# Performance work log

Hardware: AMD Instinct MI355X
Metric: run time of the kernel (lower is better)

## Reference

```python
import jax, jax.numpy as jnp
import numpy as np

B, S, D, H = 2, 2048, 1024, 16
DK = D // H

def setup_inputs() -> dict:
    key = jax.random.key(0)
    ks = jax.random.split(key, 12)
    def lin(k):
        kw, kb = jax.random.split(k)
        bound = 1.0 / np.sqrt(D)
        W = jax.random.uniform(kw, (D, D), jnp.float32, -bound, bound)
        b = jax.random.uniform(kb, (D,), jnp.float32, -bound, bound)
        return W, b
    Wq, bq = lin(ks[0]); Wk, bk = lin(ks[1]); Wv, bv = lin(ks[2]); Wo, bo = lin(ks[3])
    q = jax.random.normal(ks[4], (B, S, D), jnp.float32)
    k = jax.random.normal(ks[5], (B, S, D), jnp.float32)
    v = jax.random.normal(ks[6], (B, S, D), jnp.float32)
    mask = jnp.ones((1, 1, S, S), jnp.int32)
    return {"q": q, "k": k, "v": v, "mask": mask,
            "Wq": Wq, "bq": bq, "Wk": Wk, "bk": bk,
            "Wv": Wv, "bv": bv, "Wo": Wo, "bo": bo}

def reference(q, k, v, mask, Wq, bq, Wk, bk, Wv, bv, Wo, bo):
    # torch Linear: y = x @ W.T + b
    Q = (q @ Wq.T + bq).reshape(B, S, H, DK).transpose(0, 2, 1, 3)  # [B,H,S,DK]
    K = (k @ Wk.T + bk).reshape(B, S, H, DK).transpose(0, 2, 1, 3)
    V = (v @ Wv.T + bv).reshape(B, S, H, DK).transpose(0, 2, 1, 3)
    scores = jnp.einsum('bhqd,bhkd->bhqk', Q, K) / jnp.sqrt(jnp.float32(DK))
    scores = jnp.where(mask == 0, jnp.float32(-1e9), scores)
    attn = jax.nn.softmax(scores, axis=-1)
    context = jnp.einsum('bhqk,bhkd->bhqd', attn, V)  # [B,H,S,DK]
    concat = context.transpose(0, 2, 1, 3).reshape(B, S, D)
    return concat @ Wo.T + bo
```

## Files before the change

### kernel.cpp

```cpp
#include <hip/hip_runtime.h>
#include <hip/hip_bf16.h>

#define BB 2
#define SS 2048
#define DD 1024
#define HH 16
#define DKK 64

typedef __hip_bfloat16 bf16;
typedef unsigned short u16;
using frag_ab = __attribute__((ext_vector_type(8))) short;
using frag_cd = __attribute__((ext_vector_type(4))) float;

__device__ inline u16 f2bf(float f) {
    bf16 h = __float2bfloat16(f);
    return *reinterpret_cast<u16*>(&h);
}

__device__ inline void gld16(const void* g, void* l) {
    __builtin_amdgcn_global_load_lds((const __attribute__((address_space(1))) void*)g,
                                     (__attribute__((address_space(3))) void*)l,
                                     16, 0, 0);
}

__device__ inline int swz16(int idx) {
    return idx ^ (((idx >> 6) & 7) << 3);
}

__global__ __launch_bounds__(256) void prep(
    const float* __restrict__ q, const float* __restrict__ k, const float* __restrict__ v,
    const float* __restrict__ Wq, const float* __restrict__ Wk,
    const float* __restrict__ Wv, const float* __restrict__ Wo,
    u16* __restrict__ qb, u16* __restrict__ kb, u16* __restrict__ vb,
    u16* __restrict__ Wqb, u16* __restrict__ Wkb, u16* __restrict__ Wvb, u16* __restrict__ Wob,
    const int* __restrict__ mask, int* __restrict__ flags) {
    int bid = blockIdx.x;
    int t = threadIdx.x;
    if (bid < 8192) {
        const float* src;
        u16* dst;
        int local;
        if (bid < 6144) {
            int ts = bid >> 11;
            local = bid & 2047;
            src = ts == 0 ? q : (ts == 1 ? k : v);
            dst = ts == 0 ? qb : (ts == 1 ? kb : vb);
        } else {
            int wsel = (bid - 6144) >> 9;
            local = (bid - 6144) & 511;
            src = wsel == 0 ? Wq : (wsel == 1 ? Wk : (wsel == 2 ? Wv : Wo));
            dst = wsel == 0 ? Wqb : (wsel == 1 ? Wkb : (wsel == 2 ? Wvb : Wob));
        }
        size_t base = (size_t)local * 2048 + t * 8;
        float4 a = *(const float4*)&src[base];
        float4 b = *(const float4*)&src[base + 4];
        ushort4 u0, u1;
        u0.x = f2bf(a.x); u0.y = f2bf(a.y); u0.z = f2bf(a.z); u0.w = f2bf(a.w);
        u1.x = f2bf(b.x); u1.y = f2bf(b.y); u1.z = f2bf(b.z); u1.w = f2bf(b.w);
        *(ushort4*)&dst[base] = u0;
        *(ushort4*)&dst[base + 4] = u1;
    } else {
        int tile = bid - 8192;
        int qt = tile >> 5, kt = tile & 31;
        __shared__ int f;
        if (t == 0) f = 0;
        __syncthreads();
        int qq = qt * 64 + (t >> 2);
        const int4* row = (const int4*)(mask + (size_t)qq * SS + kt * 64 + (t & 3) * 16);
        int anyz = 0;
#pragma unroll
        for (int i = 0; i < 4; ++i) {
            int4 m4 = row[i];
            anyz |= (m4.x == 0) | (m4.y == 0) | (m4.z == 0) | (m4.w == 0);
        }
        if (anyz) f = 1;
        __syncthreads();
        if (t == 0) flags[tile] = f;
    }
}

__global__ __launch_bounds__(256) void qkv_gemm(
    const u16* __restrict__ Aq, const u16* __restrict__ Ak, const u16* __restrict__ Av,
    const u16* __restrict__ Wq, const u16* __restrict__ Wk, const u16* __restrict__ Wv,
    const float* __restrict__ bq, const float* __restrict__ bk, const float* __restrict__ bv,
    u16* __restrict__ Qo, u16* __restrict__ Ko, u16* __restrict__ Vo) {
    __shared__ u16 As[128 * 32];
    __shared__ u16 Bs[128 * 32];

    int z = blockIdx.z;
    const u16* A = z == 0 ? Aq : (z == 1 ? Ak : Av);
    const u16* W = z == 0 ? Wq : (z == 1 ? Wk : Wv);
    const float* bias = z == 0 ? bq : (z == 1 ? bk : bv);
    u16* out = z == 0 ? Qo : (z == 1 ? Ko : Vo);

    int t = threadIdx.x;
    int m0 = blockIdx.y * 128;
    int n0 = blockIdx.x * 128;
    int w = t >> 6, lane = t & 63;
    int quad = lane >> 4, l16 = lane & 15;
    int wm = w >> 1, wn = w & 1;

    const u16* Ab = A + (size_t)m0 * DD;
    const u16* Wb = W + (size_t)n0 * DD;

    frag_cd acc[4][4];
#pragma unroll
    for (int mt = 0; mt < 4; ++mt)
#pragma unroll
        for (int nt = 0; nt < 4; ++nt) acc[mt][nt] = frag_cd{0.f, 0.f, 0.f, 0.f};

    for (int k0 = 0; k0 < DD; k0 += 32) {
        if (k0) __syncthreads();
#pragma unroll
        for (int i = 0; i < 2; ++i) {
            int c = t + i * 256;
            int row = c >> 2, kc = (c & 3) * 8;
            gld16(Ab + (size_t)row * DD + k0 + kc, &As[c * 8]);
            gld16(Wb + (size_t)row * DD + k0 + kc, &Bs[c * 8]);
        }
        __syncthreads();

        frag_ab af[4], bfr[4];
#pragma unroll
        for (int mt = 0; mt < 4; ++mt)
            af[mt] = *(const frag_ab*)&As[(wm * 64 + mt * 16 + l16) * 32 + quad * 8];
#pragma unroll
        for (int nt = 0; nt < 4; ++nt)
            bfr[nt] = *(const frag_ab*)&Bs[(wn * 64 + nt * 16 + l16) * 32 + quad * 8];
#pragma unroll
        for (int mt = 0; mt < 4; ++mt)
#pragma unroll
            for (int nt = 0; nt < 4; ++nt)
                acc[mt][nt] = __builtin_amdgcn_mfma_f32_16x16x32_bf16(
                    af[mt], bfr[nt], acc[mt][nt], 0, 0, 0);
    }

    float scale = z == 0 ? 0.18033688f : 1.0f;
#pragma unroll
    for (int nt = 0; nt < 4; ++nt) {
        int n = n0 + wn * 64 + nt * 16 + l16;
        float bv_ = bias[n];
        int h_ = n >> 6, d_ = n & 63;
#pragma unroll
        for (int mt = 0; mt < 4; ++mt) {
            int mb = m0 + wm * 64 + mt * 16 + quad * 4;
            int b_ = mb >> 11, s_ = mb & 2047;
            if (z == 2) {
                ushort4 u;
                u.x = f2bf(acc[mt][nt][0] + bv_);
                u.y = f2bf(acc[mt][nt][1] + bv_);
                u.z = f2bf(acc[mt][nt][2] + bv_);
                u.w = f2bf(acc[mt][nt][3] + bv_);
                *(ushort4*)&out[((size_t)(b_ * HH + h_) * DKK + d_) * SS + s_] = u;
            } else {
#pragma unroll
                for (int r = 0; r < 4; ++r)
                    out[((size_t)(b_ * HH + h_) * SS + s_ + r) * DKK + d_] =
                        f2bf((acc[mt][nt][r] + bv_) * scale);
            }
        }
    }
}

__global__ __launch_bounds__(256) void out_gemm(const u16* __restrict__ A,
                                                const u16* __restrict__ W,
                                                const float* __restrict__ bias,
                                                float* __restrict__ out) {
    __shared__ u16 As[128 * 32];
    __shared__ u16 Bs[128 * 32];

    int t = threadIdx.x;
    int m0 = blockIdx.y * 128;
    int n0 = blockIdx.x * 128;
    int w = t >> 6, lane = t & 63;
    int quad = lane >> 4, l16 = lane & 15;
    int wm = w >> 1, wn = w & 1;

    const u16* Ab = A + (size_t)m0 * DD;
    const u16* Wb = W + (size_t)n0 * DD;

    frag_cd acc[4][4];
#pragma unroll
    for (int mt = 0; mt < 4; ++mt)
#pragma unroll
        for (int nt = 0; nt < 4; ++nt) acc[mt][nt] = frag_cd{0.f, 0.f, 0.f, 0.f};

    for (int k0 = 0; k0 < DD; k0 += 32) {
        if (k0) __syncthreads();
#pragma unroll
        for (int i = 0; i < 2; ++i) {
            int c = t + i * 256;
            int row = c >> 2, kc = (c & 3) * 8;
            gld16(Ab + (size_t)row * DD + k0 + kc, &As[c * 8]);
            gld16(Wb + (size_t)row * DD + k0 + kc, &Bs[c * 8]);
        }
        __syncthreads();

        frag_ab af[4], bfr[4];
#pragma unroll
        for (int mt = 0; mt < 4; ++mt)
            af[mt] = *(const frag_ab*)&As[(wm * 64 + mt * 16 + l16) * 32 + quad * 8];
#pragma unroll
        for (int nt = 0; nt < 4; ++nt)
            bfr[nt] = *(const frag_ab*)&Bs[(wn * 64 + nt * 16 + l16) * 32 + quad * 8];
#pragma unroll
        for (int mt = 0; mt < 4; ++mt)
#pragma unroll
            for (int nt = 0; nt < 4; ++nt)
                acc[mt][nt] = __builtin_amdgcn_mfma_f32_16x16x32_bf16(
                    af[mt], bfr[nt], acc[mt][nt], 0, 0, 0);
    }

#pragma unroll
    for (int nt = 0; nt < 4; ++nt) {
        int n = n0 + wn * 64 + nt * 16 + l16;
        float bv_ = bias[n];
#pragma unroll
        for (int mt = 0; mt < 4; ++mt) {
            int mb = m0 + wm * 64 + mt * 16 + quad * 4;
#pragma unroll
            for (int r = 0; r < 4; ++r)
                out[(size_t)(mb + r) * DD + n] = acc[mt][nt][r] + bv_;
        }
    }
}

__global__ __launch_bounds__(512) void attn_mfma(const u16* __restrict__ Qb,
                                                 const u16* __restrict__ Kb,
                                                 const u16* __restrict__ Vb,
                                                 const int* __restrict__ mask,
                                                 const int* __restrict__ flags,
                                                 u16* __restrict__ C) {
    __shared__ u16 Ks[64 * 64];
    __shared__ u16 Vt[64 * 64];
    __shared__ u16 Pw[8][16 * 72];

    int blk = blockIdx.x;
    int Qt = blk & 15;
    int bh = blk >> 4;
    int h = bh & 15;
    int b = bh >> 4;
    int q0 = Qt * 128;

    const u16* Kg = Kb + (size_t)bh * SS * DKK;
    const u16* Vg = Vb + (size_t)bh * DKK * SS;

    int t = threadIdx.x;
    int w = t >> 6;
    int lane = t & 63;
    int quad = lane >> 4;
    int l16 = lane & 15;

    frag_ab bq0, bq1;
    {
        const u16* Qr = Qb + ((size_t)bh * SS + q0 + w * 16 + l16) * DKK;
        bq0 = *(const frag_ab*)&Qr[quad * 8];
        bq1 = *(const frag_ab*)&Qr[32 + quad * 8];
    }

    frag_cd o[4];
#pragma unroll
    for (int dt = 0; dt < 4; ++dt) o[dt] = frag_cd{0.f, 0.f, 0.f, 0.f};
    float m_prev = -1e30f;
    float l_run = 0.f;

    int vd = t >> 3;
    int vc = (t & 7) * 8;
    int fbase = (Qt * 2 + (w >> 2)) * 32;

    int4 kr0, vr0;
    {
        kr0 = ((const int4*)Kg)[t];
        vr0 = *(const int4*)(Vg + (size_t)vd * SS + vc);
    }

    for (int kt = 0; kt < 32; ++kt) {
        if (kt) __syncthreads();
        *(int4*)&Ks[swz16(8 * t)] = kr0;
        *(int4*)&Vt[swz16(vd * 64 + vc)] = vr0;
        if (kt < 31) {
            kr0 = ((const int4*)(Kg + (size_t)(kt + 1) * 4096))[t];
            vr0 = *(const int4*)(Vg + (size_t)vd * SS + (kt + 1) * 64 + vc);
        }
        int az = flags[fbase + kt];
        __syncthreads();

        float s[4][4];
#pragma unroll
        for (int nt = 0; nt < 4; ++nt) {
            int kr = nt * 16 + l16;
            frag_ab ak0 = *(const frag_ab*)&Ks[swz16(kr * 64 + quad * 8)];
            frag_ab ak1 = *(const frag_ab*)&Ks[swz16(kr * 64 + 32 + quad * 8)];
            frag_cd sf = frag_cd{0.f, 0.f, 0.f, 0.f};
            sf = __builtin_amdgcn_mfma_f32_16x16x32_bf16(ak0, bq0, sf, 0, 0, 0);
            sf = __builtin_amdgcn_mfma_f32_16x16x32_bf16(ak1, bq1, sf, 0, 0, 0);
#pragma unroll
            for (int r = 0; r < 4; ++r) s[nt][r] = sf[r];
        }

        if (az) {
            int qg = q0 + w * 16 + l16;
#pragma unroll
            for (int nt = 0; nt < 4; ++nt)
#pragma unroll
                for (int r = 0; r < 4; ++r) {
                    int kg = kt * 64 + nt * 16 + quad * 4 + r;
                    if (mask[(size_t)qg * SS + kg] == 0) s[nt][r] = -1e9f;
                }
        }

        float mc = s[0][0];
#pragma unroll
        for (int nt = 0; nt < 4; ++nt)
#pragma unroll
            for (int r = 0; r < 4; ++r) mc = fmaxf(mc, s[nt][r]);
        mc = fmaxf(mc, __shfl_xor(mc, 16));
        mc = fmaxf(mc, __shfl_xor(mc, 32));
        float mnew = fmaxf(m_prev, mc);
        float alpha = exp2f(m_prev - mnew);

        float p[4][4];
        float ls = 0.f;
#pragma unroll
        for (int nt = 0; nt < 4; ++nt)
#pragma unroll
            for (int r = 0; r < 4; ++r) {
                p[nt][r] = exp2f(s[nt][r] - mnew);
                ls += p[nt][r];
            }
        ls += __shfl_xor(ls, 16);
        ls += __shfl_xor(ls, 32);
        l_run = l_run * alpha + ls;
        m_prev = mnew;

#pragma unroll
        for (int dt = 0; dt < 4; ++dt)
#pragma unroll
            for (int r = 0; r < 4; ++r) o[dt][r] *= alpha;

#pragma unroll
        for (int nt = 0; nt < 4; ++nt) {
            ushort4 up;
            up.x = f2bf(p[nt][0]); up.y = f2bf(p[nt][1]);
            up.z = f2bf(p[nt][2]); up.w = f2bf(p[nt][3]);
            *(ushort4*)&Pw[w][l16 * 72 + nt * 16 + quad * 4] = up;
        }
        frag_ab bp0 = *(const frag_ab*)&Pw[w][l16 * 72 + quad * 8];
        frag_ab bp1 = *(const frag_ab*)&Pw[w][l16 * 72 + 32 + quad * 8];

#pragma unroll
        for (int dt = 0; dt < 4; ++dt) {
            int dr = dt * 16 + l16;
            frag_ab av0 = *(const frag_ab*)&Vt[swz16(dr * 64 + quad * 8)];
            frag_ab av1 = *(const frag_ab*)&Vt[swz16(dr * 64 + 32 + quad * 8)];
            o[dt] = __builtin_amdgcn_mfma_f32_16x16x32_bf16(av0, bp0, o[dt], 0, 0, 0);
            o[dt] = __builtin_amdgcn_mfma_f32_16x16x32_bf16(av1, bp1, o[dt], 0, 0, 0);
        }
    }

    {
        float inv = 1.f / l_run;
        int qg = q0 + w * 16 + l16;
        u16* Crow = C + ((size_t)b * SS + qg) * DD + h * 64;
#pragma unroll
        for (int dt = 0; dt < 4; ++dt) {
            ushort4 u;
            u.x = f2bf(o[dt][0] * inv);
            u.y = f2bf(o[dt][1] * inv);
            u.z = f2bf(o[dt][2] * inv);
            u.w = f2bf(o[dt][3] * inv);
            *(ushort4*)&Crow[dt * 16 + quad * 4] = u;
        }
    }
}

extern "C" void kernel_launch(void* const* d_in, const int* in_sizes, int n_in,
                              void* d_out, int out_size, void* d_ws, size_t ws_size,
                              hipStream_t stream) {
    const float* q = (const float*)d_in[0];
    const float* k = (const float*)d_in[1];
    const float* v = (const float*)d_in[2];
    const int* mask = (const int*)d_in[3];
    const float* Wq = (const float*)d_in[4];
    const float* bq = (const float*)d_in[5];
    const float* Wk = (const float*)d_in[6];
    const float* bk = (const float*)d_in[7];
    const float* Wv = (const float*)d_in[8];
    const float* bv = (const float*)d_in[9];
    const float* Wo = (const float*)d_in[10];
    const float* bo = (const float*)d_in[11];
    float* out = (float*)d_out;

    const size_t MB = 1024u * 1024u;
    char* ws = (char*)d_ws;
    u16* qb = (u16*)(ws + 0 * MB);
    u16* kb = (u16*)(ws + 8 * MB);
    u16* vb = (u16*)(ws + 16 * MB);
    u16* Wqb = (u16*)(ws + 24 * MB);
    u16* Wkb = (u16*)(ws + 26 * MB);
    u16* Wvb = (u16*)(ws + 28 * MB);
    u16* Wob = (u16*)(ws + 30 * MB);
    u16* Qb = (u16*)(ws + 32 * MB);
    u16* Kb = (u16*)(ws + 40 * MB);
    u16* Vb = (u16*)(ws + 48 * MB);
    int* flags = (int*)(ws + 56 * MB);
    u16* Cw = qb;

    prep<<<9216, 256, 0, stream>>>(q, k, v, Wq, Wk, Wv, Wo,
                                   qb, kb, vb, Wqb, Wkb, Wvb, Wob, mask, flags);

    dim3 grid(DD / 128, (BB * SS) / 128, 3);
    qkv_gemm<<<grid, 256, 0, stream>>>(qb, kb, vb, Wqb, Wkb, Wvb,
                                       bq, bk, bv, Qb, Kb, Vb);

    attn_mfma<<<BB * HH * (SS / 128), 512, 0, stream>>>(Qb, Kb, Vb, mask, flags, Cw);

    out_gemm<<<dim3(DD / 128, (BB * SS) / 128), 256, 0, stream>>>(Cw, Wob, bo, out);
}
```

Baseline: 263.4 us.

## Process 128-key tiles per attention iteration with lazy softmax rescaling

Doubles the key/value tile handled per loop iteration from 64 to 128, halving barrier and loop overhead, with a new swizzle for the wider V tile. Adds a conditional online-softmax rescale that only updates the running max when the new max exceeds the old by a threshold, skipping the alpha multiply most of the time. Adds s_setprio around the MFMA blocks to favour matrix issue. Uses more LDS and registers per block, which may reduce occupancy. Reusing the P scratch buffer across the two halves relies on wave-local ordering.

```diff
diff --git a/kernel.cpp b/kernel.cpp
--- a/kernel.cpp
+++ b/kernel.cpp
@@ -25,6 +25,9 @@
 
 __device__ inline int swz16(int idx) {
     return idx ^ (((idx >> 6) & 7) << 3);
+}
+__device__ inline int swzV(int idx) {
+    return idx ^ (((idx >> 7) & 7) << 3);
 }
 
 __global__ __launch_bounds__(256) void prep(
@@ -231,8 +234,8 @@
                                                  const int* __restrict__ mask,
                                                  const int* __restrict__ flags,
                                                  u16* __restrict__ C) {
-    __shared__ u16 Ks[64 * 64];
-    __shared__ u16 Vt[64 * 64];
+    __shared__ u16 Ks[128 * 64];
+    __shared__ u16 Vt[64 * 128];
     __shared__ u16 Pw[8][16 * 72];
 
     int blk = blockIdx.x;
@@ -264,30 +267,39 @@
     float m_prev = -1e30f;
     float l_run = 0.f;
 
-    int vd = t >> 3;
-    int vc = (t & 7) * 8;
+    int vrow = t >> 4;
+    int vcol = (t & 15) * 8;
     int fbase = (Qt * 2 + (w >> 2)) * 32;
 
-    int4 kr0, vr0;
+    int4 kr0, kr1, vr0, vr1;
     {
         kr0 = ((const int4*)Kg)[t];
-        vr0 = *(const int4*)(Vg + (size_t)vd * SS + vc);
-    }
-
-    for (int kt = 0; kt < 32; ++kt) {
-        if (kt) __syncthreads();
+        kr1 = ((const int4*)Kg)[t + 512];
+        vr0 = *(const int4*)(Vg + (size_t)vrow * SS + vcol);
+        vr1 = *(const int4*)(Vg + (size_t)(vrow + 32) * SS + vcol);
+    }
+
+    for (int s2 = 0; s2 < 16; ++s2) {
+        if (s2) __syncthreads();
         *(int4*)&Ks[swz16(8 * t)] = kr0;
-        *(int4*)&Vt[swz16(vd * 64 + vc)] = vr0;
-        if (kt < 31) {
-            kr0 = ((const int4*)(Kg + (size_t)(kt + 1) * 4096))[t];
-            vr0 = *(const int4*)(Vg + (size_t)vd * SS + (kt + 1) * 64 + vc);
-        }
-        int az = flags[fbase + kt];
+        *(int4*)&Ks[swz16(8 * (t + 512))] = kr1;
+        *(int4*)&Vt[swzV(vrow * 128 + vcol)] = vr0;
+        *(int4*)&Vt[swzV((vrow + 32) * 128 + vcol)] = vr1;
+        if (s2 < 15) {
+            const int4* Kt = (const int4*)(Kg + (size_t)(s2 + 1) * 8192);
+            kr0 = Kt[t];
+            kr1 = Kt[t + 512];
+            vr0 = *(const int4*)(Vg + (size_t)vrow * SS + (s2 + 1) * 128 + vcol);
+            vr1 = *(const int4*)(Vg + (size_t)(vrow + 32) * SS + (s2 + 1) * 128 + vcol);
+        }
+        int az0 = flags[fbase + 2 * s2];
+        int az1 = flags[fbase + 2 * s2 + 1];
         __syncthreads();
 
-        float s[4][4];
-#pragma unroll
-        for (int nt = 0; nt < 4; ++nt) {
+        float sc[8][4];
+        __builtin_amdgcn_s_setprio(1);
+#pragma unroll
+        for (int nt = 0; nt < 8; ++nt) {
             int kr = nt * 16 + l16;
             frag_ab ak0 = *(const frag_ab*)&Ks[swz16(kr * 64 + quad * 8)];
             frag_ab ak1 = *(const frag_ab*)&Ks[swz16(kr * 64 + 32 + quad * 8)];
@@ -295,66 +307,77 @@
             sf = __builtin_amdgcn_mfma_f32_16x16x32_bf16(ak0, bq0, sf, 0, 0, 0);
             sf = __builtin_amdgcn_mfma_f32_16x16x32_bf16(ak1, bq1, sf, 0, 0, 0);
 #pragma unroll
-            for (int r = 0; r < 4; ++r) s[nt][r] = sf[r];
-        }
-
-        if (az) {
+            for (int r = 0; r < 4; ++r) sc[nt][r] = sf[r];
+        }
+        __builtin_amdgcn_s_setprio(0);
+
+        if (az0 | az1) {
             int qg = q0 + w * 16 + l16;
 #pragma unroll
-            for (int nt = 0; nt < 4; ++nt)
-#pragma unroll
-                for (int r = 0; r < 4; ++r) {
-                    int kg = kt * 64 + nt * 16 + quad * 4 + r;
-                    if (mask[(size_t)qg * SS + kg] == 0) s[nt][r] = -1e9f;
+            for (int nt = 0; nt < 8; ++nt) {
+                if (nt < 4 ? az0 : az1) {
+#pragma unroll
+                    for (int r = 0; r < 4; ++r) {
+                        int kg = s2 * 128 + nt * 16 + quad * 4 + r;
+                        if (mask[(size_t)qg * SS + kg] == 0) sc[nt][r] = -1e9f;
+                    }
                 }
-        }
-
-        float mc = s[0][0];
-#pragma unroll
-        for (int nt = 0; nt < 4; ++nt)
-#pragma unroll
-            for (int r = 0; r < 4; ++r) mc = fmaxf(mc, s[nt][r]);
+            }
+        }
+
+        float mc = sc[0][0];
+#pragma unroll
+        for (int nt = 0; nt < 8; ++nt)
+#pragma unroll
+            for (int r = 0; r < 4; ++r) mc = fmaxf(mc, sc[nt][r]);
         mc = fmaxf(mc, __shfl_xor(mc, 16));
         mc = fmaxf(mc, __shfl_xor(mc, 32));
-        float mnew = fmaxf(m_prev, mc);
-        float alpha = exp2f(m_prev - mnew);
-
-        float p[4][4];
+        if (!__all(mc <= m_prev + 11.f)) {
+            float mnew = fmaxf(m_prev, mc);
+            float alpha = exp2f(m_prev - mnew);
+            l_run *= alpha;
+#pragma unroll
+            for (int dt = 0; dt < 4; ++dt)
+#pragma unroll
+                for (int r = 0; r < 4; ++r) o[dt][r] *= alpha;
+            m_prev = mnew;
+        }
+
         float ls = 0.f;
 #pragma unroll
-        for (int nt = 0; nt < 4; ++nt)
+        for (int nt = 0; nt < 8; ++nt)
 #pragma unroll
             for (int r = 0; r < 4; ++r) {
-                p[nt][r] = exp2f(s[nt][r] - mnew);
-                ls += p[nt][r];
+                sc[nt][r] = exp2f(sc[nt][r] - m_prev);
+                ls += sc[nt][r];
             }
         ls += __shfl_xor(ls, 16);
         ls += __shfl_xor(ls, 32);
-        l_run = l_run * alpha + ls;
-        m_prev = mnew;
-
-#pragma unroll
-        for (int dt = 0; dt < 4; ++dt)
-#pragma unroll
-            for (int r = 0; r < 4; ++r) o[dt][r] *= alpha;
-
-#pragma unroll
-        for (int nt = 0; nt < 4; ++nt) {
-            ushort4 up;
-            up.x = f2bf(p[nt][0]); up.y = f2bf(p[nt][1]);
-            up.z = f2bf(p[nt][2]); up.w = f2bf(p[nt][3]);
-            *(ushort4*)&Pw[w][l16 * 72 + nt * 16 + quad * 4] = up;
-        }
-        frag_ab bp0 = *(const frag_ab*)&Pw[w][l16 * 72 + quad * 8];
-        frag_ab bp1 = *(const frag_ab*)&Pw[w][l16 * 72 + 32 + quad * 8];
-
-#pragma unroll
-        for (int dt = 0; dt < 4; ++dt) {
-            int dr = dt * 16 + l16;
-            frag_ab av0 = *(const frag_ab*)&Vt[swz16(dr * 64 + quad * 8)];
-            frag_ab av1 = *(const frag_ab*)&Vt[swz16(dr * 64 + 32 + quad * 8)];
-            o[dt] = __builtin_amdgcn_mfma_f32_16x16x32_bf16(av0, bp0, o[dt], 0, 0, 0);
-            o[dt] = __builtin_amdgcn_mfma_f32_16x16x32_bf16(av1, bp1, o[dt], 0, 0, 0);
+        l_run += ls;
+
+#pragma unroll
+        for (int hh = 0; hh < 2; ++hh) {
+#pragma unroll
+            for (int j = 0; j < 4; ++j) {
+                int nt = hh * 4 + j;
+                ushort4 up;
+                up.x = f2bf(sc[nt][0]); up.y = f2bf(sc[nt][1]);
+                up.z = f2bf(sc[nt][2]); up.w = f2bf(sc[nt][3]);
+                *(ushort4*)&Pw[w][l16 * 72 + j * 16 + quad * 4] = up;
+            }
+            frag_ab bp0 = *(const frag_ab*)&Pw[w][l16 * 72 + quad * 8];
+            frag_ab bp1 = *(const frag_ab*)&Pw[w][l16 * 72 + 32 + quad * 8];
+
+            __builtin_amdgcn_s_setprio(1);
+#pragma unroll
+            for (int dt = 0; dt < 4; ++dt) {
+                int dr = dt * 16 + l16;
+                frag_ab av0 = *(const frag_ab*)&Vt[swzV(dr * 128 + hh * 64 + quad * 8)];
+                frag_ab av1 = *(const frag_ab*)&Vt[swzV(dr * 128 + hh * 64 + 32 + quad * 8)];
+                o[dt] = __builtin_amdgcn_mfma_f32_16x16x32_bf16(av0, bp0, o[dt], 0, 0, 0);
+                o[dt] = __builtin_amdgcn_mfma_f32_16x16x32_bf16(av1, bp1, o[dt], 0, 0, 0);
+            }
+            __builtin_amdgcn_s_setprio(0);
         }
     }
 
```

New measurement: 276.2 us. +4.9%, slower.
